# Optimization experiments

Measured on AMD Instinct MI355X. Metric: run time of the kernel, lower is better.

## Reference

```python
import jax, jax.numpy as jnp
import numpy as np

B = 32          # batch
IH = IW = 32    # image_size
N = IH * IW     # tokens = 1024
INP = 256
OUP = 256
H = 8           # heads
D = 32          # dim_head
INNER = H * D   # 256
TABLE = (2 * IH - 1) * (2 * IW - 1)  # 3969


def _rel_index():
    # exact replica of the torch buffer construction
    coords = np.stack(np.meshgrid(np.arange(IH), np.arange(IW), indexing='ij')).reshape(2, -1)
    rel = coords[:, :, None] - coords[:, None, :]
    rel[0] += IH - 1
    rel[1] += IW - 1
    rel[0] *= 2 * IW - 1
    return (rel[0] + rel[1]).reshape(-1)  # [N*N]


def setup_inputs() -> dict:
    key = jax.random.key(0)
    k0, k1, k2, k3 = jax.random.split(key, 4)
    x = jax.random.normal(k0, (B, N, INP), jnp.float32)
    W_qkv = jax.random.normal(k1, (INP, 3 * INNER), jnp.float32) * 0.02
    bias_table = jax.random.normal(k2, (TABLE, H), jnp.float32) * 0.02
    W_out = jax.random.normal(k3, (INNER, OUP), jnp.float32) * 0.02
    b_out = jnp.zeros((OUP,), jnp.float32)
    rel_index = jnp.asarray(_rel_index(), jnp.int32)
    return {"x": x, "W_qkv": W_qkv, "bias_table": bias_table,
            "W_out": W_out, "b_out": b_out, "rel_index": rel_index}


def reference(x, W_qkv, bias_table, W_out, b_out, rel_index):
    scale = D ** -0.5
    qkv = x @ W_qkv                                   # [B, N, 3*INNER]
    q, k, v = jnp.split(qkv, 3, axis=-1)
    to_heads = lambda t: t.reshape(B, N, H, D).transpose(0, 2, 1, 3)  # b h n d
    q, k, v = to_heads(q), to_heads(k), to_heads(v)
    dots = jnp.einsum('bhid,bhjd->bhij', q, k) * scale  # [B, H, N, N]
    # gather per-head relative position bias: [N*N, H] -> [1, H, N, N]
    bias = bias_table[rel_index].reshape(N, N, H).transpose(2, 0, 1)[None]
    attn = jax.nn.softmax(dots + bias, axis=-1)
    out = jnp.einsum('bhij,bhjd->bhid', attn, v)        # [B, H, N, D]
    out = out.transpose(0, 2, 1, 3).reshape(B, N, INNER)
    return out @ W_out + b_out
```

## Files before the change

### kernel.cpp

```cpp
#include <hip/hip_runtime.h>

typedef __attribute__((ext_vector_type(4))) int            vi4;
typedef __attribute__((ext_vector_type(4))) float          vf4;
typedef __attribute__((ext_vector_type(8))) short          vs8;
typedef __attribute__((ext_vector_type(4))) short          vs4;
typedef __attribute__((ext_vector_type(2))) unsigned int   vu2;
typedef unsigned short u16;
typedef unsigned int   u32;

#define LOG2E  1.4426950408889634f
#define QSCALE 0.2550484109f

static __device__ __forceinline__ u16 f2bf(float f) {
  u32 u = __builtin_bit_cast(u32, f);
  u32 r = (u + 0x7fffu + ((u >> 16) & 1u)) >> 16;
  return (u16)r;
}
static __device__ __forceinline__ float bfu_lo(u32 u) {
  return __builtin_bit_cast(float, u << 16);
}
static __device__ __forceinline__ float bfu_hi(u32 u) {
  return __builtin_bit_cast(float, u & 0xffff0000u);
}
static __device__ __forceinline__ u32 packbf_perm(float a, float b) {
  return __builtin_amdgcn_perm(__builtin_bit_cast(u32, b),
                               __builtin_bit_cast(u32, a), 0x07060302u);
}
static __device__ __forceinline__ vf4 unpack_bias(const u32* grp, int tj) {
  u32 b0 = grp[tj * 2], b1 = grp[tj * 2 + 1];
  vf4 c; c[0] = bfu_lo(b0); c[1] = bfu_hi(b0);
  c[2] = bfu_lo(b1); c[3] = bfu_hi(b1);
  return c;
}
static __device__ __forceinline__ float exp2_raw(float x) {
#if __has_builtin(__builtin_amdgcn_exp2f)
  return __builtin_amdgcn_exp2f(x);
#else
  float r;
  asm("v_exp_f32 %0, %1" : "=v"(r) : "v"(x));
  return r;
#endif
}

static __device__ __forceinline__ void ldsdma16(void* lds, const void* g) {
  __builtin_amdgcn_global_load_lds(
      (const u32 __attribute__((address_space(1)))*)g,
      (u32 __attribute__((address_space(3)))*)lds, 16, 0, 0);
}

__global__ void prep_all(const float* __restrict__ x, u16* __restrict__ xbf,
                         const float* __restrict__ Wqkv, u16* __restrict__ WqkvT,
                         const float* __restrict__ Wout, u16* __restrict__ WoutT,
                         const int* __restrict__ rel, const float* __restrict__ table,
                         u32* __restrict__ bias_pk, float* __restrict__ bias_f,
                         int use_f32) {
  __shared__ __align__(8) u16 relS[64 * 32];
  int bid = blockIdx.x, tid = threadIdx.x;
  if (bid < 4096) {
    int i = (bid * 256 + tid) * 8;
    vf4 v0 = *(const vf4*)&x[i];
    vf4 v1 = *(const vf4*)&x[i + 4];
    vi4 o;
    o[0] = (int)((u32)f2bf(v0[0]) | ((u32)f2bf(v0[1]) << 16));
    o[1] = (int)((u32)f2bf(v0[2]) | ((u32)f2bf(v0[3]) << 16));
    o[2] = (int)((u32)f2bf(v1[0]) | ((u32)f2bf(v1[1]) << 16));
    o[3] = (int)((u32)f2bf(v1[2]) | ((u32)f2bf(v1[3]) << 16));
    *(vi4*)&xbf[i] = o;
  } else if (bid < 5120) {
    const float* src; u16* dst; int C, idx;
    if (bid < 4864) { src = Wqkv; dst = WqkvT; C = 768; idx = (bid - 4096) * 256 + tid; }
    else            { src = Wout; dst = WoutT; C = 256; idx = (bid - 4864) * 256 + tid; }
    int r = idx / C, c = idx - r * C;
    dst[c * 256 + r] = f2bf(src[idx]);
  } else {
    int b2 = bid - 5120;
    int qt = b2 >> 6, t = (b2 >> 2) & 15, s = b2 & 3;
    int ti = s >> 1, jhalf = s & 1;
    int wave = tid >> 6, quad = (tid >> 4) & 3, l15 = tid & 15;
    int jbase = t * 64 + jhalf * 32;

#pragma unroll
    for (int p = 0; p < 2; ++p) {
      int task = p * 256 + tid;
      int q = task >> 3, unit = task & 7;
      int m = qt * 128 + (q >> 4) * 32 + ti * 16 + (q & 15);
      vi4 v = *(const vi4*)&rel[m * 1024 + jbase + unit * 4];
      vu2 pk;
      pk[0] = (u32)(v[0] & 0xffff) | ((u32)v[1] << 16);
      pk[1] = (u32)(v[2] & 0xffff) | ((u32)v[3] << 16);
      *(vu2*)&relS[q * 32 + unit * 4] = pk;
    }
    __syncthreads();

    int mrow = wave * 16 + l15;
    float vals[8][8];
#pragma unroll
    for (int tjl = 0; tjl < 2; ++tjl)
#pragma unroll
      for (int r = 0; r < 4; ++r) {
        int idx = relS[mrow * 32 + tjl * 16 + quad * 4 + r];
        vf4 a = *(const vf4*)&table[idx * 8];
        vf4 bb = *(const vf4*)&table[idx * 8 + 4];
#pragma unroll
        for (int h = 0; h < 4; ++h) {
          vals[tjl * 4 + r][h] = a[h];
          vals[tjl * 4 + r][h + 4] = bb[h];
        }
      }
    if (use_f32) {
#pragma unroll
      for (int h = 0; h < 8; ++h)
#pragma unroll
        for (int tjl = 0; tjl < 2; ++tjl) {
          int frag = ti * 4 + jhalf * 2 + tjl;
          vf4 v;
#pragma unroll
          for (int r = 0; r < 4; ++r) v[r] = vals[tjl * 4 + r][h] * LOG2E;
          *(vf4*)&bias_f[(((h * 8 + qt) * 16 + t) * 8 + frag) * 1024 + tid * 4] = v;
        }
    } else {
#pragma unroll
      for (int h = 0; h < 8; ++h) {
        u32 o[4];
#pragma unroll
        for (int tjl = 0; tjl < 2; ++tjl)
#pragma unroll
          for (int p = 0; p < 2; ++p) {
            u32 lo = f2bf(vals[tjl * 4 + 2 * p][h] * LOG2E);
            u32 hi = f2bf(vals[tjl * 4 + 2 * p + 1][h] * LOG2E);
            o[tjl * 2 + p] = lo | (hi << 16);
          }
        *(vi4*)&bias_pk[h * 524288 + (qt * 16 + t) * 4096 + s * 1024 + tid * 4] =
            *(const vi4*)o;
      }
    }
  }
}

template <int EPI>
__global__ __launch_bounds__(256, 4) void gemm_k256(
    const u16* __restrict__ A, const u16* __restrict__ Bt,
    u16* __restrict__ q_out, u16* __restrict__ k_out, u16* __restrict__ v_out,
    float* __restrict__ c_out, const float* __restrict__ bias) {
  __shared__ __align__(16) u16 SMEM[EPI == 0 ? 128 * 136 : 16384];
  const int tid = threadIdx.x;
  const int lane15 = tid & 15, quad = (tid >> 4) & 3, wave = tid >> 6;
  const int wr = (wave & 1) * 64, wc = (wave >> 1) * 64;
  const int bid = blockIdx.x;
  const int w = bid >> 3;
  const int m0 = (((bid & 7) << 5) + (w & 31)) * 128;
  const int n0 = (w >> 5) * 128;

  const u16* Ag = &A[(m0 + (tid >> 2)) * 256 + (tid & 3) * 8];
  const u16* Bg = &Bt[(n0 + (tid >> 2)) * 256 + (tid & 3) * 8];
  u16* AsW0 = &SMEM[wave * 512];
  u16* BsW0 = &SMEM[4096 + wave * 512];
  u16* AsW1 = &SMEM[8192 + wave * 512];
  u16* BsW1 = &SMEM[12288 + wave * 512];

  const vf4 z4 = {0.f, 0.f, 0.f, 0.f};
  vf4 acc[4][4];
#pragma unroll
  for (int i = 0; i < 4; ++i)
#pragma unroll
    for (int j = 0; j < 4; ++j) acc[i][j] = z4;

  ldsdma16(AsW0,        Ag);
  ldsdma16(AsW0 + 2048, Ag + 64 * 256);
  ldsdma16(BsW0,        Bg);
  ldsdma16(BsW0 + 2048, Bg + 64 * 256);

#define G_TILE(KS, CUR)                                                        \
  do {                                                                         \
    if ((KS) < 7) {                                                            \
      u16* da = (CUR) ? AsW0 : AsW1;          \
      u16* db = (CUR) ? BsW0 : BsW1;                                           \
      ldsdma16(da,        Ag + ((KS) + 1) * 32);                               \
      ldsdma16(da + 2048, Ag + ((KS) + 1) * 32 + 64 * 256);                    \
      ldsdma16(db,        Bg + ((KS) + 1) * 32);                               \
      ldsdma16(db + 2048, Bg + ((KS) + 1) * 32 + 64 * 256);                    \
      asm volatile("s_waitcnt vmcnt(4)" ::: "memory");                         \
    } else {                                                                   \
      asm volatile("s_waitcnt vmcnt(0)" ::: "memory");                         \
    }                                                                          \
    __builtin_amdgcn_sched_barrier(0);                                         \
    __builtin_amdgcn_s_barrier();          \
    __builtin_amdgcn_sched_barrier(0);                                         \
    {                                                                          \
      const u16* Ab = (CUR) ? &SMEM[8192] : &SMEM[0];                          \
      const u16* Bb = Ab + 4096;                                               \
      vs8 af[4], bfr[4];                                                       \
      _Pragma("unroll")                                                        \
      for (int ti = 0; ti < 4; ++ti)                                           \
        af[ti] = *(const vs8*)&Ab[(wr + ti * 16 + lane15) * 32 + quad * 8];    \
      _Pragma("unroll")                                                        \
      for (int tj = 0; tj < 4; ++tj)                                           \
        bfr[tj] = *(const vs8*)&Bb[(wc + tj * 16 + lane15) * 32 + quad * 8];   \
      _Pragma("unroll")                                                        \
      for (int ti = 0; ti < 4; ++ti)                                           \
        _Pragma("unroll")                                                      \
        for (int tj = 0; tj < 4; ++tj)                                         \
          acc[ti][tj] = __builtin_amdgcn_mfma_f32_16x16x32_bf16(               \
              af[ti], bfr[tj], acc[ti][tj], 0, 0, 0);                          \
    }                                                                          \
    __builtin_amdgcn_sched_barrier(0);                                         \
    __builtin_amdgcn_s_barrier();        \
  } while (0)

#pragma unroll
  for (int kk = 0; kk < 8; kk += 2) {
    G_TILE(kk, 0);
    G_TILE(kk + 1, 1);
  }
#undef G_TILE

  if (EPI == 0) {
    const int which = n0 >> 8;
    const int bb = m0 >> 10, nn0 = m0 & 1023;
    u16* Cs = SMEM;
    __syncthreads();
    if (which < 2) {
      float sc = (which == 0) ? QSCALE : 1.f;
#pragma unroll
      for (int tj = 0; tj < 4; ++tj) {
        int col = wc + tj * 16 + lane15;
#pragma unroll
        for (int ti = 0; ti < 4; ++ti) {
          int row0 = wr + ti * 16 + quad * 4;
#pragma unroll
          for (int r = 0; r < 4; ++r)
            Cs[(row0 + r) * 136 + col] = f2bf(acc[ti][tj][r] * sc);
        }
      }
      __syncthreads();
      u16* base = (which == 0) ? q_out : k_out;
#pragma unroll
      for (int hp = 0; hp < 4; ++hp) {
        int hh = ((n0 + hp * 32) >> 5) & 7;
        u16* pb = base + ((bb * 8 + hh) * 1024 + nn0) * 32;
#pragma unroll
        for (int p2 = 0; p2 < 2; ++p2) {
          int task = p2 * 256 + tid;
          int row = task >> 2, unit = task & 3;
          vi4 v = *(const vi4*)&Cs[row * 136 + hp * 32 + unit * 8];
          *(vi4*)&pb[row * 32 + unit * 8] = v;
        }
      }
    } else {
#pragma unroll
      for (int tj = 0; tj < 4; ++tj) {
        int col = wc + tj * 16 + lane15;
#pragma unroll
        for (int ti = 0; ti < 4; ++ti) {
          int row0 = wr + ti * 16 + quad * 4;
          vu2 pk;
          pk[0] = (u32)f2bf(acc[ti][tj][0]) | ((u32)f2bf(acc[ti][tj][1]) << 16);
          pk[1] = (u32)f2bf(acc[ti][tj][2]) | ((u32)f2bf(acc[ti][tj][3]) << 16);
          *(vu2*)&Cs[col * 136 + row0] = pk;
        }
      }
      __syncthreads();
#pragma unroll
      for (int p = 0; p < 8; ++p) {
        int task = p * 256 + tid;
        int col = task >> 4, unit = task & 15;
        int cg = n0 + col;
        int hh = (cg >> 5) & 7, d = cg & 31;
        vi4 v = *(const vi4*)&Cs[col * 136 + unit * 8];
        *(vi4*)&v_out[((bb * 8 + hh) * 32 + d) * 1024 + nn0 + unit * 8] = v;
      }
    }
  } else {
#pragma unroll
    for (int tj = 0; tj < 4; ++tj) {
      int colg = n0 + wc + tj * 16 + lane15;
      float bo = bias[colg];
#pragma unroll
      for (int ti = 0; ti < 4; ++ti)
#pragma unroll
        for (int r = 0; r < 4; ++r) {
          int rowg = m0 + wr + ti * 16 + quad * 4 + r;
          c_out[rowg * 256 + colg] = acc[ti][tj][r] + bo;
        }
    }
  }
}

__global__ __launch_bounds__(256, 4) void gemm_out(
    const u16* __restrict__ A, const u16* __restrict__ Bt,
    float* __restrict__ c_out, const float* __restrict__ bias) {
  __shared__ __align__(16) u16 SMEM[12288];
  const int tid = threadIdx.x;
  const int lane15 = tid & 15, quad = (tid >> 4) & 3, wave = tid >> 6;
  const int bid = blockIdx.x;
  const int mt = ((bid & 7) << 6) + ((bid >> 3) & 63);
  const int m0 = mt * 64;
  const int n0 = (bid >> 9) << 7;

  const u16* Ag = &A[(m0 + (tid >> 2)) * 256 + (tid & 3) * 8];
  const u16* Bg = &Bt[(n0 + (tid >> 2)) * 256 + (tid & 3) * 8];
  u16* AsW0 = &SMEM[wave * 512];
  u16* BsW0 = &SMEM[2048 + wave * 512];
  u16* AsW1 = &SMEM[6144 + wave * 512];
  u16* BsW1 = &SMEM[8192 + wave * 512];

  const vf4 z4 = {0.f, 0.f, 0.f, 0.f};
  vf4 acc[4][2];
#pragma unroll
  for (int i = 0; i < 4; ++i) {
    acc[i][0] = z4; acc[i][1] = z4;
  }

  ldsdma16(AsW0,        Ag);
  ldsdma16(BsW0,        Bg);
  ldsdma16(BsW0 + 2048, Bg + 64 * 256);

#define GO_TILE(KS, CUR)                                                       \
  do {                                                                         \
    if ((KS) < 7) {                                                            \
      u16* da = (CUR) ? AsW0 : AsW1;                                           \
      u16* db = (CUR) ? BsW0 : BsW1;                                           \
      ldsdma16(da,        Ag + ((KS) + 1) * 32);                               \
      ldsdma16(db,        Bg + ((KS) + 1) * 32);                               \
      ldsdma16(db + 2048, Bg + ((KS) + 1) * 32 + 64 * 256);                    \
      asm volatile("s_waitcnt vmcnt(3)" ::: "memory");                         \
    } else {                                                                   \
      asm volatile("s_waitcnt vmcnt(0)" ::: "memory");                         \
    }                                                                          \
    __builtin_amdgcn_sched_barrier(0);                                         \
    __builtin_amdgcn_s_barrier();                                              \
    __builtin_amdgcn_sched_barrier(0);                                         \
    {                                                                          \
      const u16* Ab = (CUR) ? &SMEM[6144] : &SMEM[0];                          \
      const u16* Bb = Ab + 2048;                                               \
      vs8 af[4], bfr[2];                                                       \
      _Pragma("unroll")                                                        \
      for (int ti = 0; ti < 4; ++ti)                                           \
        af[ti] = *(const vs8*)&Ab[(ti * 16 + lane15) * 32 + quad * 8];         \
      _Pragma("unroll")                                                        \
      for (int tj = 0; tj < 2; ++tj)                                           \
        bfr[tj] = *(const vs8*)&Bb[(wave * 32 + tj * 16 + lane15) * 32         \
                                   + quad * 8];                                \
      _Pragma("unroll")                                                        \
      for (int ti = 0; ti < 4; ++ti)                                           \
        _Pragma("unroll")                                                      \
        for (int tj = 0; tj < 2; ++tj)                                         \
          acc[ti][tj] = __builtin_amdgcn_mfma_f32_16x16x32_bf16(               \
              af[ti], bfr[tj], acc[ti][tj], 0, 0, 0);                          \
    }                                                                          \
    __builtin_amdgcn_sched_barrier(0);                                         \
    __builtin_amdgcn_s_barrier();                                              \
  } while (0)

#pragma unroll
  for (int kk = 0; kk < 8; kk += 2) {
    GO_TILE(kk, 0);
    GO_TILE(kk + 1, 1);
  }
#undef GO_TILE

#pragma unroll
  for (int tj = 0; tj < 2; ++tj) {
    int colg = n0 + wave * 32 + tj * 16 + lane15;
    float bo = bias[colg];
#pragma unroll
    for (int ti = 0; ti < 4; ++ti)
#pragma unroll
      for (int r = 0; r < 4; ++r) {
        int rowg = m0 + ti * 16 + quad * 4 + r;
        c_out[rowg * 256 + colg] = acc[ti][tj][r] + bo;
      }
  }
}

template <int BF32>
__global__ __launch_bounds__(256, 4) void flash_attn(
    const u16* __restrict__ Qws, const u16* __restrict__ Kws,
    const u16* __restrict__ Vtws, const void* __restrict__ biasv,
    u16* __restrict__ Ows) {
  __shared__ __align__(16) u16 Ks[2][64 * 40];
  __shared__ __align__(16) u16 Vt[2][32 * 72];

  const int tid = threadIdx.x;
  const int l15 = tid & 15, quad = (tid >> 4) & 3, wave = tid >> 6;
  const int bid = blockIdx.x;
  const int h = bid & 7, b = (bid >> 3) & 31, qt = bid >> 8;
  const int q0 = qt * 128;
  const int bh = b * 8 + h;
  const u16* Qbase = Qws + (bh * 1024 + q0) * 32;
  const u16* Kbase = Kws + bh * 1024 * 32;
  const u16* Vbase = Vtws + bh * 32 * 1024;
  const float* Bf = (const float*)biasv + (h * 8 + qt) * 131072 + tid * 4;
  const u32*  Bpk = (const u32*)biasv + h * 524288 + qt * 65536 + tid * 4;

  const int kv_j = tid >> 2, kv_seg = (tid & 3) * 8;
  const int v_d = tid >> 3,  v_seg = (tid & 7) * 8;
  const u16* Kg = Kbase + kv_j * 32 + kv_seg;
  const u16* Vg = Vbase + v_d * 1024 + v_seg;

  vs8 af[2];
#pragma unroll
  for (int ti = 0; ti < 2; ++ti)
    af[ti] = *(const vs8*)&Qbase[(wave * 32 + ti * 16 + l15) * 32 + quad * 8];

  vi4 kreg = *(const vi4*)Kg;
  vi4 vreg = *(const vi4*)Vg;
  *(vi4*)&Ks[0][kv_j * 40 + kv_seg] = kreg;
  *(vi4*)&Vt[0][v_d * 72 + v_seg] = vreg;

  vf4 b0pre[4];
  vi4 bpk_pre[2];
  if (BF32) {
#pragma unroll
    for (int i = 0; i < 4; ++i) b0pre[i] = *(const vf4*)&Bf[i * 1024];
  } else {
#pragma unroll
    for (int i = 0; i < 2; ++i) bpk_pre[i] = *(const vi4*)(Bpk + i * 1024);
  }

  const vf4 z4 = {0.f, 0.f, 0.f, 0.f};
  vf4 O[2][2];
  O[0][0] = z4; O[0][1] = z4; O[1][0] = z4; O[1][1] = z4;
  vf4 Lacc[2];
  Lacc[0] = z4; Lacc[1] = z4;

  vs4 ones4;
#pragma unroll
  for (int i = 0; i < 4; ++i) ones4[i] = (short)0x3F80;

  const int ks_off = l15 * 40 + quad * 8;
  const int vt_off = l15 * 72 + quad * 4;

#define FA_TILE(T, CUR)                                                        \
  do {                                                                         \
    __syncthreads();                 \
          \
                                 \
    vf4 b1cur[4];                                                              \
    vi4 bpk1[2];                                                               \
    if (BF32) {                                                                \
      _Pragma("unroll")                                                        \
      for (int i = 0; i < 4; ++i)                                              \
        b1cur[i] = *(const vf4*)&Bf[((T) * 8 + 4 + i) * 1024];                 \
    } else {                                                                   \
      bpk1[0] = *(const vi4*)(Bpk + (T) * 4096 + 2048);                        \
      bpk1[1] = *(const vi4*)(Bpk + (T) * 4096 + 3072);                        \
    }                                                                          \
    if ((T) < 15) {                                                            \
      kreg = *(const vi4*)(Kg + ((T) + 1) * 2048);                             \
      vreg = *(const vi4*)(Vg + ((T) + 1) * 64);                               \
    }                                                                          \
    __builtin_amdgcn_s_setprio(1);                                             \
    _Pragma("unroll")                                                          \
    for (int tj = 0; tj < 4; ++tj) {                                           \
      vs8 bk = *(const vs8*)&Ks[CUR][tj * 640 + ks_off];                       \
      vs4 va0 = *(const vs4*)&Vt[CUR][vt_off + tj * 16];                       \
      vs4 va1 = *(const vs4*)&Vt[CUR][vt_off + 1152 + tj * 16];                \
      _Pragma("unroll")                                                        \
      for (int ti = 0; ti < 2; ++ti) {                                         \
        vf4 c = BF32 ? (ti ? b1cur[tj] : b0pre[tj])                            \
                     : unpack_bias((const u32*)(ti ? bpk1 : bpk_pre), tj);     \
        vf4 st = __builtin_amdgcn_mfma_f32_16x16x32_bf16(bk, af[ti], c,        \
                                                         0, 0, 0);             \
        float p0 = exp2_raw(st[0]);                                            \
        float p1 = exp2_raw(st[1]);                                            \
        float p2 = exp2_raw(st[2]);                                            \
        float p3 = exp2_raw(st[3]);                                            \
        vu2 pw; pw[0] = packbf_perm(p0, p1); pw[1] = packbf_perm(p2, p3);      \
        vs4 pf = __builtin_bit_cast(vs4, pw);                                  \
        O[ti][0] = __builtin_amdgcn_mfma_f32_16x16x16bf16_1k(va0, pf,          \
                                                             O[ti][0], 0, 0, 0); \
        O[ti][1] = __builtin_amdgcn_mfma_f32_16x16x16bf16_1k(va1, pf,          \
                                                             O[ti][1], 0, 0, 0); \
        Lacc[ti] = __builtin_amdgcn_mfma_f32_16x16x16bf16_1k(ones4, pf,        \
                                                             Lacc[ti], 0, 0, 0); \
      }                                                                        \
    }                                                                          \
    __builtin_amdgcn_s_setprio(0);                                             \
       \
    if ((T) < 15) {                                                            \
      *(vi4*)&Ks[(CUR) ^ 1][kv_j * 40 + kv_seg] = kreg;                        \
      *(vi4*)&Vt[(CUR) ^ 1][v_d * 72 + v_seg] = vreg;                          \
      if (BF32) {                                                              \
        _Pragma("unroll")                                                      \
        for (int i = 0; i < 4; ++i)                                            \
          b0pre[i] = *(const vf4*)&Bf[(((T) + 1) * 8 + i) * 1024];             \
      } else {                                                                 \
        bpk_pre[0] = *(const vi4*)(Bpk + ((T) + 1) * 4096);                    \
        bpk_pre[1] = *(const vi4*)(Bpk + ((T) + 1) * 4096 + 1024);             \
      }                                                                        \
    }                                                                          \
  } while (0)

  for (int tt = 0; tt < 16; tt += 2) {
    FA_TILE(tt, 0);
    FA_TILE(tt + 1, 1);
  }
#undef FA_TILE

#pragma unroll
  for (int ti = 0; ti < 2; ++ti) {
    float inv = __builtin_amdgcn_rcpf(Lacc[ti][0]);
    int m = q0 + wave * 32 + ti * 16 + l15;
    int rowbase = (b * 1024 + m) * 256 + h * 32;
#pragma unroll
    for (int tj2 = 0; tj2 < 2; ++tj2) {
      u32 lo = (u32)f2bf(O[ti][tj2][0] * inv) | ((u32)f2bf(O[ti][tj2][1] * inv) << 16);
      u32 hi = (u32)f2bf(O[ti][tj2][2] * inv) | ((u32)f2bf(O[ti][tj2][3] * inv) << 16);
      vu2 pk; pk[0] = lo; pk[1] = hi;
      *(vu2*)&Ows[rowbase + tj2 * 16 + quad * 4] = pk;
    }
  }
}

extern "C" void kernel_launch(void* const* d_in, const int* in_sizes, int n_in,
                              void* d_out, int out_size, void* d_ws, size_t ws_size,
                              hipStream_t stream) {
  (void)in_sizes; (void)n_in; (void)out_size;
  const float* x     = (const float*)d_in[0];
  const float* Wqkv  = (const float*)d_in[1];
  const float* table = (const float*)d_in[2];
  const float* Wout  = (const float*)d_in[3];
  const float* bout  = (const float*)d_in[4];
  const int*   rel   = (const int*)d_in[5];
  float* out = (float*)d_out;

  const int use_f32 = 0;
  const size_t bias_bytes = 16777216ull;

  char* ws = (char*)d_ws;
  u16* xbf    = (u16*)(ws);
  u16* Qws    = (u16*)(ws + 16777216);
  u16* Kws    = (u16*)(ws + 33554432);
  u16* Vtws   = (u16*)(ws + 50331648);
  void* biasp = (void*)(ws + 67108864);
  u16* WqkvT  = (u16*)(ws + 67108864 + bias_bytes);
  u16* WoutT  = WqkvT + 196608;

  prep_all<<<5632, 256, 0, stream>>>(x, xbf, Wqkv, WqkvT, Wout, WoutT,
                                     rel, table, (u32*)biasp, (float*)biasp,
                                     use_f32);
  gemm_k256<0><<<1536, 256, 0, stream>>>(xbf, WqkvT, Qws, Kws, Vtws,
                                         nullptr, nullptr);
  flash_attn<0><<<2048, 256, 0, stream>>>(Qws, Kws, Vtws, biasp, xbf);
  gemm_out<<<1024, 256, 0, stream>>>(xbf, WoutT, out, bout);
}
```

Measured before the change: 188.8 us.

## Fuse x fp32-to-bf16 conversion into QKV GEMM and co-launch bias gather

The separate pass that converted x to bf16 is removed. The QKV GEMM now loads fp32 x into registers, converts it and writes bf16 into LDS inside its pipelined k-loop, so a full write and re-read of the bf16 x buffer is avoided. The relative-bias gather blocks are moved out of the prep kernel and appended as extra blocks of the QKV GEMM launch, so they run alongside it. The trade-offs are twice the global read bytes for the A operand, register-staged loads in place of direct LDS DMA, and an extra lgkmcnt wait plus LDS stores in each k-step.

```diff
diff --git a/kernel.cpp b/kernel.cpp
--- a/kernel.cpp
+++ b/kernel.cpp
@@ -31,6 +31,14 @@
   vf4 c; c[0] = bfu_lo(b0); c[1] = bfu_hi(b0);
   c[2] = bfu_lo(b1); c[3] = bfu_hi(b1);
   return c;
+}
+static __device__ __forceinline__ vi4 cvt8(vf4 a, vf4 b) {
+  vi4 o;
+  o[0] = (int)((u32)f2bf(a[0]) | ((u32)f2bf(a[1]) << 16));
+  o[1] = (int)((u32)f2bf(a[2]) | ((u32)f2bf(a[3]) << 16));
+  o[2] = (int)((u32)f2bf(b[0]) | ((u32)f2bf(b[1]) << 16));
+  o[3] = (int)((u32)f2bf(b[2]) | ((u32)f2bf(b[3]) << 16));
+  return o;
 }
 static __device__ __forceinline__ float exp2_raw(float x) {
 #if __has_builtin(__builtin_amdgcn_exp2f)
@@ -48,36 +56,32 @@
       (u32 __attribute__((address_space(3)))*)lds, 16, 0, 0);
 }
 
-__global__ void prep_all(const float* __restrict__ x, u16* __restrict__ xbf,
-                         const float* __restrict__ Wqkv, u16* __restrict__ WqkvT,
-                         const float* __restrict__ Wout, u16* __restrict__ WoutT,
-                         const int* __restrict__ rel, const float* __restrict__ table,
-                         u32* __restrict__ bias_pk, float* __restrict__ bias_f,
-                         int use_f32) {
-  __shared__ __align__(8) u16 relS[64 * 32];
+__global__ void prep_w(const float* __restrict__ Wqkv, u16* __restrict__ WqkvT,
+                       const float* __restrict__ Wout, u16* __restrict__ WoutT) {
   int bid = blockIdx.x, tid = threadIdx.x;
-  if (bid < 4096) {
-    int i = (bid * 256 + tid) * 8;
-    vf4 v0 = *(const vf4*)&x[i];
-    vf4 v1 = *(const vf4*)&x[i + 4];
-    vi4 o;
-    o[0] = (int)((u32)f2bf(v0[0]) | ((u32)f2bf(v0[1]) << 16));
-    o[1] = (int)((u32)f2bf(v0[2]) | ((u32)f2bf(v0[3]) << 16));
-    o[2] = (int)((u32)f2bf(v1[0]) | ((u32)f2bf(v1[1]) << 16));
-    o[3] = (int)((u32)f2bf(v1[2]) | ((u32)f2bf(v1[3]) << 16));
-    *(vi4*)&xbf[i] = o;
-  } else if (bid < 5120) {
-    const float* src; u16* dst; int C, idx;
-    if (bid < 4864) { src = Wqkv; dst = WqkvT; C = 768; idx = (bid - 4096) * 256 + tid; }
-    else            { src = Wout; dst = WoutT; C = 256; idx = (bid - 4864) * 256 + tid; }
-    int r = idx / C, c = idx - r * C;
-    dst[c * 256 + r] = f2bf(src[idx]);
-  } else {
-    int b2 = bid - 5120;
+  const float* src; u16* dst; int C, idx;
+  if (bid < 768) { src = Wqkv; dst = WqkvT; C = 768; idx = bid * 256 + tid; }
+  else           { src = Wout; dst = WoutT; C = 256; idx = (bid - 768) * 256 + tid; }
+  int r = idx / C, c = idx - r * C;
+  dst[c * 256 + r] = f2bf(src[idx]);
+}
+
+__global__ __launch_bounds__(256, 4) void gemm_qkv_bias(
+    const float* __restrict__ x, const u16* __restrict__ Bt,
+    u16* __restrict__ q_out, u16* __restrict__ k_out, u16* __restrict__ v_out,
+    const int* __restrict__ rel, const float* __restrict__ table,
+    u32* __restrict__ bias_pk) {
+  __shared__ __align__(16) u16 SMEM[128 * 136];
+  const int tid = threadIdx.x;
+  const int bid = blockIdx.x;
+
+  if (bid >= 1536) {
+    int b2 = bid - 1536;
     int qt = b2 >> 6, t = (b2 >> 2) & 15, s = b2 & 3;
     int ti = s >> 1, jhalf = s & 1;
     int wave = tid >> 6, quad = (tid >> 4) & 3, l15 = tid & 15;
     int jbase = t * 64 + jhalf * 32;
+    u16* relS = SMEM;
 
 #pragma unroll
     for (int p = 0; p < 2; ++p) {
@@ -107,55 +111,34 @@
           vals[tjl * 4 + r][h + 4] = bb[h];
         }
       }
-    if (use_f32) {
-#pragma unroll
-      for (int h = 0; h < 8; ++h)
-#pragma unroll
-        for (int tjl = 0; tjl < 2; ++tjl) {
-          int frag = ti * 4 + jhalf * 2 + tjl;
-          vf4 v;
-#pragma unroll
-          for (int r = 0; r < 4; ++r) v[r] = vals[tjl * 4 + r][h] * LOG2E;
-          *(vf4*)&bias_f[(((h * 8 + qt) * 16 + t) * 8 + frag) * 1024 + tid * 4] = v;
+#pragma unroll
+    for (int h = 0; h < 8; ++h) {
+      u32 o[4];
+#pragma unroll
+      for (int tjl = 0; tjl < 2; ++tjl)
+#pragma unroll
+        for (int p = 0; p < 2; ++p) {
+          u32 lo = f2bf(vals[tjl * 4 + 2 * p][h] * LOG2E);
+          u32 hi = f2bf(vals[tjl * 4 + 2 * p + 1][h] * LOG2E);
+          o[tjl * 2 + p] = lo | (hi << 16);
         }
-    } else {
-#pragma unroll
-      for (int h = 0; h < 8; ++h) {
-        u32 o[4];
-#pragma unroll
-        for (int tjl = 0; tjl < 2; ++tjl)
-#pragma unroll
-          for (int p = 0; p < 2; ++p) {
-            u32 lo = f2bf(vals[tjl * 4 + 2 * p][h] * LOG2E);
-            u32 hi = f2bf(vals[tjl * 4 + 2 * p + 1][h] * LOG2E);
-            o[tjl * 2 + p] = lo | (hi << 16);
-          }
-        *(vi4*)&bias_pk[h * 524288 + (qt * 16 + t) * 4096 + s * 1024 + tid * 4] =
-            *(const vi4*)o;
-      }
-    }
-  }
-}
-
-template <int EPI>
-__global__ __launch_bounds__(256, 4) void gemm_k256(
-    const u16* __restrict__ A, const u16* __restrict__ Bt,
-    u16* __restrict__ q_out, u16* __restrict__ k_out, u16* __restrict__ v_out,
-    float* __restrict__ c_out, const float* __restrict__ bias) {
-  __shared__ __align__(16) u16 SMEM[EPI == 0 ? 128 * 136 : 16384];
-  const int tid = threadIdx.x;
+      *(vi4*)&bias_pk[h * 524288 + (qt * 16 + t) * 4096 + s * 1024 + tid * 4] =
+          *(const vi4*)o;
+    }
+    return;
+  }
+
   const int lane15 = tid & 15, quad = (tid >> 4) & 3, wave = tid >> 6;
   const int wr = (wave & 1) * 64, wc = (wave >> 1) * 64;
-  const int bid = blockIdx.x;
   const int w = bid >> 3;
   const int m0 = (((bid & 7) << 5) + (w & 31)) * 128;
   const int n0 = (w >> 5) * 128;
 
-  const u16* Ag = &A[(m0 + (tid >> 2)) * 256 + (tid & 3) * 8];
+  const float* Ax = &x[(m0 + (tid >> 2)) * 256 + (tid & 3) * 8];
   const u16* Bg = &Bt[(n0 + (tid >> 2)) * 256 + (tid & 3) * 8];
-  u16* AsW0 = &SMEM[wave * 512];
+  u16* AsD0 = &SMEM[tid * 8];
+  u16* AsD1 = &SMEM[8192 + tid * 8];
   u16* BsW0 = &SMEM[4096 + wave * 512];
-  u16* AsW1 = &SMEM[8192 + wave * 512];
   u16* BsW1 = &SMEM[12288 + wave * 512];
 
   const vf4 z4 = {0.f, 0.f, 0.f, 0.f};
@@ -165,26 +148,37 @@
 #pragma unroll
     for (int j = 0; j < 4; ++j) acc[i][j] = z4;
 
-  ldsdma16(AsW0,        Ag);
-  ldsdma16(AsW0 + 2048, Ag + 64 * 256);
-  ldsdma16(BsW0,        Bg);
-  ldsdma16(BsW0 + 2048, Bg + 64 * 256);
-
-#define G_TILE(KS, CUR)                                                        \
+  {
+    vf4 p0 = *(const vf4*)Ax;
+    vf4 p1 = *(const vf4*)(Ax + 4);
+    vf4 p2 = *(const vf4*)(Ax + 64 * 256);
+    vf4 p3 = *(const vf4*)(Ax + 64 * 256 + 4);
+    ldsdma16(BsW0,        Bg);
+    ldsdma16(BsW0 + 2048, Bg + 64 * 256);
+    *(vi4*)AsD0 = cvt8(p0, p1);
+    *(vi4*)(AsD0 + 2048) = cvt8(p2, p3);
+  }
+
+#define GQ_TILE(KS, CUR)                                                       \
   do {                                                                         \
+    vf4 a0, a1, a2, a3;                                                        \
     if ((KS) < 7) {                                                            \
-      u16* da = (CUR) ? AsW0 : AsW1;          \
+      const float* ax = Ax + ((KS) + 1) * 32;                                  \
+      a0 = *(const vf4*)ax;                                                    \
+      a1 = *(const vf4*)(ax + 4);                                              \
+      a2 = *(const vf4*)(ax + 64 * 256);                                       \
+      a3 = *(const vf4*)(ax + 64 * 256 + 4);                                   \
       u16* db = (CUR) ? BsW0 : BsW1;                                           \
-      ldsdma16(da,        Ag + ((KS) + 1) * 32);                               \
-      ldsdma16(da + 2048, Ag + ((KS) + 1) * 32 + 64 * 256);                    \
       ldsdma16(db,        Bg + ((KS) + 1) * 32);                               \
       ldsdma16(db + 2048, Bg + ((KS) + 1) * 32 + 64 * 256);                    \
-      asm volatile("s_waitcnt vmcnt(4)" ::: "memory");                         \
+      __builtin_amdgcn_sched_barrier(0);                                       \
+      asm volatile("s_waitcnt vmcnt(6)" ::: "memory");                         \
     } else {                                                                   \
       asm volatile("s_waitcnt vmcnt(0)" ::: "memory");                         \
     }                                                                          \
-    __builtin_amdgcn_sched_barrier(0);                                         \
-    __builtin_amdgcn_s_barrier();          \
+    asm volatile("s_waitcnt lgkmcnt(0)" ::: "memory");                         \
+    __builtin_amdgcn_sched_barrier(0);                                         \
+    __builtin_amdgcn_s_barrier();                        \
     __builtin_amdgcn_sched_barrier(0);                                         \
     {                                                                          \
       const u16* Ab = (CUR) ? &SMEM[8192] : &SMEM[0];                          \
@@ -204,84 +198,75 @@
               af[ti], bfr[tj], acc[ti][tj], 0, 0, 0);                          \
     }                                                                          \
     __builtin_amdgcn_sched_barrier(0);                                         \
+    if ((KS) < 7) {                                                            \
+      u16* ad = (CUR) ? AsD0 : AsD1;               \
+      *(vi4*)ad = cvt8(a0, a1);                                                \
+      *(vi4*)(ad + 2048) = cvt8(a2, a3);                                       \
+    }                                                                          \
+    __builtin_amdgcn_sched_barrier(0);                                         \
     __builtin_amdgcn_s_barrier();        \
   } while (0)
 
 #pragma unroll
   for (int kk = 0; kk < 8; kk += 2) {
-    G_TILE(kk, 0);
-    G_TILE(kk + 1, 1);
-  }
-#undef G_TILE
-
-  if (EPI == 0) {
-    const int which = n0 >> 8;
-    const int bb = m0 >> 10, nn0 = m0 & 1023;
-    u16* Cs = SMEM;
+    GQ_TILE(kk, 0);
+    GQ_TILE(kk + 1, 1);
+  }
+#undef GQ_TILE
+
+  const int which = n0 >> 8;
+  const int bb = m0 >> 10, nn0 = m0 & 1023;
+  u16* Cs = SMEM;
+  __syncthreads();
+  if (which < 2) {
+    float sc = (which == 0) ? QSCALE : 1.f;
+#pragma unroll
+    for (int tj = 0; tj < 4; ++tj) {
+      int col = wc + tj * 16 + lane15;
+#pragma unroll
+      for (int ti = 0; ti < 4; ++ti) {
+        int row0 = wr + ti * 16 + quad * 4;
+#pragma unroll
+        for (int r = 0; r < 4; ++r)
+          Cs[(row0 + r) * 136 + col] = f2bf(acc[ti][tj][r] * sc);
+      }
+    }
     __syncthreads();
-    if (which < 2) {
-      float sc = (which == 0) ? QSCALE : 1.f;
-#pragma unroll
-      for (int tj = 0; tj < 4; ++tj) {
-        int col = wc + tj * 16 + lane15;
-#pragma unroll
-        for (int ti = 0; ti < 4; ++ti) {
-          int row0 = wr + ti * 16 + quad * 4;
-#pragma unroll
-          for (int r = 0; r < 4; ++r)
-            Cs[(row0 + r) * 136 + col] = f2bf(acc[ti][tj][r] * sc);
-        }
+    u16* base = (which == 0) ? q_out : k_out;
+#pragma unroll
+    for (int hp = 0; hp < 4; ++hp) {
+      int hh = ((n0 + hp * 32) >> 5) & 7;
+      u16* pb = base + ((bb * 8 + hh) * 1024 + nn0) * 32;
+#pragma unroll
+      for (int p2 = 0; p2 < 2; ++p2) {
+        int task = p2 * 256 + tid;
+        int row = task >> 2, unit = task & 3;
+        vi4 v = *(const vi4*)&Cs[row * 136 + hp * 32 + unit * 8];
+        *(vi4*)&pb[row * 32 + unit * 8] = v;
       }
-      __syncthreads();
-      u16* base = (which == 0) ? q_out : k_out;
-#pragma unroll
-      for (int hp = 0; hp < 4; ++hp) {
-        int hh = ((n0 + hp * 32) >> 5) & 7;
-        u16* pb = base + ((bb * 8 + hh) * 1024 + nn0) * 32;
-#pragma unroll
-        for (int p2 = 0; p2 < 2; ++p2) {
-          int task = p2 * 256 + tid;
-          int row = task >> 2, unit = task & 3;
-          vi4 v = *(const vi4*)&Cs[row * 136 + hp * 32 + unit * 8];
-          *(vi4*)&pb[row * 32 + unit * 8] = v;
-        }
+    }
+  } else {
+#pragma unroll
+    for (int tj = 0; tj < 4; ++tj) {
+      int col = wc + tj * 16 + lane15;
+#pragma unroll
+      for (int ti = 0; ti < 4; ++ti) {
+        int row0 = wr + ti * 16 + quad * 4;
+        vu2 pk;
+        pk[0] = (u32)f2bf(acc[ti][tj][0]) | ((u32)f2bf(acc[ti][tj][1]) << 16);
+        pk[1] = (u32)f2bf(acc[ti][tj][2]) | ((u32)f2bf(acc[ti][tj][3]) << 16);
+        *(vu2*)&Cs[col * 136 + row0] = pk;
       }
-    } else {
-#pragma unroll
-      for (int tj = 0; tj < 4; ++tj) {
-        int col = wc + tj * 16 + lane15;
-#pragma unroll
-        for (int ti = 0; ti < 4; ++ti) {
-          int row0 = wr + ti * 16 + quad * 4;
-          vu2 pk;
-          pk[0] = (u32)f2bf(acc[ti][tj][0]) | ((u32)f2bf(acc[ti][tj][1]) << 16);
-          pk[1] = (u32)f2bf(acc[ti][tj][2]) | ((u32)f2bf(acc[ti][tj][3]) << 16);
-          *(vu2*)&Cs[col * 136 + row0] = pk;
-        }
-      }
-      __syncthreads();
-#pragma unroll
-      for (int p = 0; p < 8; ++p) {
-        int task = p * 256 + tid;
-        int col = task >> 4, unit = task & 15;
-        int cg = n0 + col;
-        int hh = (cg >> 5) & 7, d = cg & 31;
-        vi4 v = *(const vi4*)&Cs[col * 136 + unit * 8];
-        *(vi4*)&v_out[((bb * 8 + hh) * 32 + d) * 1024 + nn0 + unit * 8] = v;
-      }
-    }
-  } else {
-#pragma unroll
-    for (int tj = 0; tj < 4; ++tj) {
-      int colg = n0 + wc + tj * 16 + lane15;
-      float bo = bias[colg];
-#pragma unroll
-      for (int ti = 0; ti < 4; ++ti)
-#pragma unroll
-        for (int r = 0; r < 4; ++r) {
-          int rowg = m0 + wr + ti * 16 + quad * 4 + r;
-          c_out[rowg * 256 + colg] = acc[ti][tj][r] + bo;
-        }
+    }
+    __syncthreads();
+#pragma unroll
+    for (int p = 0; p < 8; ++p) {
+      int task = p * 256 + tid;
+      int col = task >> 4, unit = task & 15;
+      int cg = n0 + col;
+      int hh = (cg >> 5) & 7, d = cg & 31;
+      vi4 v = *(const vi4*)&Cs[col * 136 + unit * 8];
+      *(vi4*)&v_out[((bb * 8 + hh) * 32 + d) * 1024 + nn0 + unit * 8] = v;
     }
   }
 }
@@ -525,11 +510,10 @@
   const int*   rel   = (const int*)d_in[5];
   float* out = (float*)d_out;
 
-  const int use_f32 = 0;
   const size_t bias_bytes = 16777216ull;
 
   char* ws = (char*)d_ws;
-  u16* xbf    = (u16*)(ws);
+  u16* Ows    = (u16*)(ws);
   u16* Qws    = (u16*)(ws + 16777216);
   u16* Kws    = (u16*)(ws + 33554432);
   u16* Vtws   = (u16*)(ws + 50331648);
@@ -537,11 +521,9 @@
   u16* WqkvT  = (u16*)(ws + 67108864 + bias_bytes);
   u16* WoutT  = WqkvT + 196608;
 
-  prep_all<<<5632, 256, 0, stream>>>(x, xbf, Wqkv, WqkvT, Wout, WoutT,
-                                     rel, table, (u32*)biasp, (float*)biasp,
-                                     use_f32);
-  gemm_k256<0><<<1536, 256, 0, stream>>>(xbf, WqkvT, Qws, Kws, Vtws,
-                                         nullptr, nullptr);
-  flash_attn<0><<<2048, 256, 0, stream>>>(Qws, Kws, Vtws, biasp, xbf);
-  gemm_out<<<1024, 256, 0, stream>>>(xbf, WoutT, out, bout);
-}
+  prep_w<<<1024, 256, 0, stream>>>(Wqkv, WqkvT, Wout, WoutT);
+  gemm_qkv_bias<<<2048, 256, 0, stream>>>(x, WqkvT, Qws, Kws, Vtws,
+                                          rel, table, (u32*)biasp);
+  flash_attn<0><<<2048, 256, 0, stream>>>(Qws, Kws, Vtws, biasp, Ows);
+  gemm_out<<<1024, 256, 0, stream>>>(Ows, WoutT, out, bout);
+}
```

New measurement: 194.0 us. 2.8% more time.
